# Performance work log

Measured on AMD Instinct MI355X. Metric: run time of the kernel, lower is better.

Reference implementation:

```python
import math
import jax, jax.numpy as jnp
import numpy as np

B, T, D_MODEL, H = 8, 2048, 1024, 16
D_HEAD = D_MODEL // H


def _rel_shift(x):
    # x: (B, T, H, H) -- faithful port of the TF pad/reshape/slice trick,
    # which in this module operates on the time axis (dim 1).
    b, t, h, h2 = x.shape
    x = jnp.pad(x, ((0, 0), (1, 0), (0, 0), (0, 0)))  # (B, T+1, H, H)
    x = x.reshape(t + 1, b, h, h2)[1:]                 # drop first row
    return x.reshape(b, t, h, h2)


def setup_inputs() -> dict:
    key = jax.random.key(0)
    ks = jax.random.split(key, 16)
    s = 1.0 / math.sqrt(D_MODEL)
    return {
        "inputs": jax.random.normal(ks[0], (B, T, D_MODEL), jnp.float32),
        "pos_embedding": jax.random.normal(ks[1], (B, T, D_MODEL), jnp.float32),
        "masks": jnp.ones((B, T), dtype=bool),
        "Wq": jax.random.normal(ks[2], (D_MODEL, D_MODEL), jnp.float32) * s,
        "bq": jnp.zeros((D_MODEL,), jnp.float32),
        "Wk": jax.random.normal(ks[3], (D_MODEL, D_MODEL), jnp.float32) * s,
        "bk": jnp.zeros((D_MODEL,), jnp.float32),
        "Wv": jax.random.normal(ks[4], (D_MODEL, D_MODEL), jnp.float32) * s,
        "bv": jnp.zeros((D_MODEL,), jnp.float32),
        "Wp": jax.random.normal(ks[5], (D_MODEL, D_MODEL), jnp.float32) * s,
        "Wo": jax.random.normal(ks[6], (D_MODEL, D_MODEL), jnp.float32) * s,
        "bo": jnp.zeros((D_MODEL,), jnp.float32),
        "u_bias": jax.random.normal(ks[7], (H, D_HEAD), jnp.float32) * 0.05,
        "v_bias": jax.random.normal(ks[8], (H, D_HEAD), jnp.float32) * 0.05,
    }


def reference(inputs, pos_embedding, masks, Wq, bq, Wk, bk, Wv, bv, Wp, Wo, bo, u_bias, v_bias):
    b, t, _ = inputs.shape
    sqrt_dim = math.sqrt(D_MODEL)
    q = (inputs @ Wq + bq).reshape(b, t, H, D_HEAD)
    k = (inputs @ Wk + bk).reshape(b, t, H, D_HEAD)
    v = (inputs @ Wv + bv).reshape(b, t, H, D_HEAD)
    p = (pos_embedding @ Wp).reshape(b, t, H, D_HEAD)

    # NOTE: no (B,H,T,D) transpose in the original -> HxH scores per timestep.
    content_score = jnp.einsum("bthd,btkd->bthk", q + u_bias, k)  # (B,T,H,H)
    pos_score = jnp.einsum("bthd,btkd->bthk", q + v_bias, p)      # (B,T,H,H)
    pos_score = _rel_shift(pos_score)
    score = (content_score + pos_score) / sqrt_dim
    score = jnp.where(masks[:, :, None, None], score, jnp.float32(1e-9))
    attn = jax.nn.softmax(score, axis=-1)
    ctx = jnp.einsum("bthk,btkd->bthd", attn, v)                  # (B,T,H,D)
    ctx = ctx.transpose(0, 2, 1, 3).reshape(b, -1, D_MODEL)       # (B,T,d_model)
    return ctx @ Wo + bo
```

## Files before the change

### kernel.cpp

```cpp
#include <hip/hip_runtime.h>


typedef __attribute__((ext_vector_type(8))) short short8;
typedef __attribute__((ext_vector_type(4))) float f32x4;

__device__ __forceinline__ ushort f2bf(float f) {
    unsigned u = __float_as_uint(f);
    u += 0x7FFFu + ((u >> 16) & 1u);
    return (ushort)(u >> 16);
}
__device__ __forceinline__ float bf2f(ushort u) {
    return __uint_as_float(((unsigned)u) << 16);
}

typedef const unsigned int __attribute__((address_space(1)))* gas_t;
typedef unsigned int __attribute__((address_space(3)))* las_t;
__device__ __forceinline__ void gl_lds16(const ushort* g, ushort* l) {
    __builtin_amdgcn_global_load_lds((gas_t)g, (las_t)l, 16, 0, 0);
}

__global__ __launch_bounds__(256)
void conv_bf16_k(const float* __restrict__ in, ushort* __restrict__ out)
{
    const size_t i = ((size_t)blockIdx.x * 256 + threadIdx.x) * 8;
    float4 a = *(const float4*)(in + i);
    float4 b = *(const float4*)(in + i + 4);
    short8 o = {(short)f2bf(a.x), (short)f2bf(a.y), (short)f2bf(a.z), (short)f2bf(a.w),
                (short)f2bf(b.x), (short)f2bf(b.y), (short)f2bf(b.z), (short)f2bf(b.w)};
    *(short8*)(out + i) = o;
}

__global__ __launch_bounds__(256)
void transpose_convert_k(const float* __restrict__ W, ushort* __restrict__ Wt, int K, int N)
{
    __shared__ float tile[32][33];
    const int tx = threadIdx.x & 31;
    const int ty = threadIdx.x >> 5;
    const int n0 = blockIdx.x * 32;
    const int k0 = blockIdx.y * 32;
#pragma unroll
    for (int i = 0; i < 4; ++i)
        tile[ty + i * 8][tx] = W[(size_t)(k0 + ty + i * 8) * N + n0 + tx];
    __syncthreads();
#pragma unroll
    for (int i = 0; i < 4; ++i)
        Wt[(size_t)(n0 + ty + i * 8) * K + k0 + tx] = f2bf(tile[tx][ty + i * 8]);
}

__global__ __launch_bounds__(256)
void bias_concat_k(const float* __restrict__ b0, const float* __restrict__ b1,
                   const float* __restrict__ b2, float* __restrict__ out)
{
    const int i = blockIdx.x * 256 + threadIdx.x;
    const int s = i >> 10;
    const int j = i & 1023;
    out[i] = (s == 0) ? b0[j] : (s == 1) ? b1[j] : b2[j];
}

#define VMC(n) asm volatile("s_waitcnt vmcnt(" #n ")" ::: "memory")

template<int HAS_BIAS, int OUT_BF16>
__global__ __launch_bounds__(512, 4)
void gemm6_k(const ushort* __restrict__ A, const ushort* __restrict__ Bt,
             const float* __restrict__ bias, void* __restrict__ Cv,
             int N, int K)
{
    __shared__ ushort As[3 * 4096];
    __shared__ ushort Bs[3 * 8192];
    const int tid = threadIdx.x;
    const int l = tid & 63;
    const int w = tid >> 6;
    const int wr = w >> 2;
    const int wc = w & 3;

    const int gx = gridDim.x;
    const int lin = blockIdx.y * gx + blockIdx.x;
    const int xcd = lin & 7;
    const int idx = lin >> 3;
    const int hb = gridDim.y >> 3;
    const int sxc = gx >> 2;
    const int g4 = idx >> 4;
    const int li = idx & 15;
    const int bx = (g4 % sxc) * 4 + (li & 3);
    const int by = xcd * hb + (g4 / sxc) * 4 + (li >> 2);
    const int bm = by * 128;
    const int bn = bx * 256;
    const int NT = K >> 5;

    const int srow = tid >> 2;
    const int scol = ((tid & 3) ^ ((tid >> 3) & 3)) * 8;
    const ushort* Ag  = A  + (size_t)(bm + srow) * K + scol;
    const ushort* Bg  = Bt + (size_t)(bn + srow) * K + scol;
    const ushort* Bg2 = Bg + (size_t)128 * K;
    const int lw = w * 512;

    const int lr = l & 15;
    const int fb = (((l >> 4) ^ ((l >> 1) & 3)) * 8);
    const int laneA = (wr * 64 + lr) * 32 + fb;
    const int laneB = (wc * 64 + lr) * 32 + fb;

    f32x4 acc[4][4];
#pragma unroll
    for (int i = 0; i < 4; ++i)
#pragma unroll
        for (int n = 0; n < 4; ++n)
            acc[i][n] = (f32x4){0.f, 0.f, 0.f, 0.f};

#define STAGE6(tt, rg) do { \
    ushort* ha = As + (rg) * 4096 + lw; \
    ushort* hbp = Bs + (rg) * 8192 + lw; \
    const size_t ko = (size_t)(tt) * 32; \
    gl_lds16(Ag + ko, ha); \
    gl_lds16(Bg + ko, hbp); \
    gl_lds16(Bg2 + ko, hbp + 4096); \
} while (0)

    STAGE6(0, 0);
    STAGE6(1, 1);
    VMC(3);
    __builtin_amdgcn_s_barrier();
    __builtin_amdgcn_sched_barrier(0);

    int cur = 0, stg = 2;
    for (int t = 0; t < NT; ++t) {
        if (t + 2 < NT) STAGE6(t + 2, stg);
        const ushort* ap = As + cur * 4096 + laneA;
        const ushort* bp = Bs + cur * 8192 + laneB;
        short8 af[4], bf4[4];
#pragma unroll
        for (int m = 0; m < 4; ++m) af[m] = *(const short8*)(ap + m * 512);
#pragma unroll
        for (int n = 0; n < 4; ++n) bf4[n] = *(const short8*)(bp + n * 512);
        asm volatile("s_waitcnt lgkmcnt(0)" ::: "memory");
        __builtin_amdgcn_sched_barrier(0);
        __builtin_amdgcn_s_setprio(1);
#pragma unroll
        for (int m = 0; m < 4; ++m)
#pragma unroll
            for (int n = 0; n < 4; ++n)
                acc[m][n] = __builtin_amdgcn_mfma_f32_16x16x32_bf16(af[m], bf4[n], acc[m][n], 0, 0, 0);
        __builtin_amdgcn_s_setprio(0);
        __builtin_amdgcn_sched_barrier(0);
        if (t < NT - 2) { VMC(3); }
        else if (t == NT - 2) { VMC(0); }
        if (t < NT - 1) {
            __builtin_amdgcn_s_barrier();
            __builtin_amdgcn_sched_barrier(0);
        }
        cur = (cur == 2) ? 0 : cur + 1;
        stg = (stg == 2) ? 0 : stg + 1;
    }
#undef STAGE6

    const int cr = (l >> 4) * 4;
    const int cc = l & 15;
    float bv[4];
#pragma unroll
    for (int n = 0; n < 4; ++n)
        bv[n] = HAS_BIAS ? bias[bn + wc * 64 + n * 16 + cc] : 0.f;
#pragma unroll
    for (int m = 0; m < 4; ++m) {
#pragma unroll
        for (int n = 0; n < 4; ++n) {
            const int col = bn + wc * 64 + n * 16 + cc;
#pragma unroll
            for (int r = 0; r < 4; ++r) {
                const int row = bm + wr * 64 + m * 16 + cr + r;
                float v = acc[m][n][r] + bv[n];
                if (OUT_BF16) ((ushort*)Cv)[(size_t)row * N + col] = f2bf(v);
                else          ((float*)Cv)[(size_t)row * N + col] = v;
            }
        }
    }
}

__global__ __launch_bounds__(256)
void attn2_k(const ushort* __restrict__ qkv, const ushort* __restrict__ pbuf,
             const float* __restrict__ ubias, const float* __restrict__ vbias,
             const int* __restrict__ masks, ushort* __restrict__ ctx)
{
    __shared__ __align__(16) float Pl[4][16 * 20];

    const int tid = threadIdx.x;
    const int w = tid >> 6;
    const int l = tid & 63;
    const int m = blockIdx.x * 4 + w;
    const int b2 = m >> 11;
    const int t2 = m & 2047;
    const int f  = m + 8;
    const int bs = f / 2049;
    const int ts = f - bs * 2049;
    const bool haspos = (ts != 0);
    const int mp = bs * 2048 + ts - 1;

    const int lr = l & 15;
    const int g  = l >> 4;
    const int ko = g * 8;

    const ushort* qb = qkv + (size_t)m * 3072;

    short8 quf[2], kf[2], qvf[2], pf[2];
#pragma unroll
    for (int c = 0; c < 2; ++c) {
        const int off = lr * 64 + c * 32 + ko;
        short8 q = *(const short8*)(qb + off);
        kf[c]    = *(const short8*)(qb + 1024 + off);
        float4 u0 = *(const float4*)(ubias + off);
        float4 u1 = *(const float4*)(ubias + off + 4);
        quf[c] = (short8){
            (short)f2bf(bf2f((ushort)q[0]) + u0.x), (short)f2bf(bf2f((ushort)q[1]) + u0.y),
            (short)f2bf(bf2f((ushort)q[2]) + u0.z), (short)f2bf(bf2f((ushort)q[3]) + u0.w),
            (short)f2bf(bf2f((ushort)q[4]) + u1.x), (short)f2bf(bf2f((ushort)q[5]) + u1.y),
            (short)f2bf(bf2f((ushort)q[6]) + u1.z), (short)f2bf(bf2f((ushort)q[7]) + u1.w)};
    }
    if (haspos) {
        const ushort* qmp = qkv + (size_t)mp * 3072;
        const ushort* pp  = pbuf + (size_t)mp * 1024;
#pragma unroll
        for (int c = 0; c < 2; ++c) {
            const int off = lr * 64 + c * 32 + ko;
            short8 q = *(const short8*)(qmp + off);
            pf[c]    = *(const short8*)(pp + off);
            float4 v0 = *(const float4*)(vbias + off);
            float4 v1 = *(const float4*)(vbias + off + 4);
            qvf[c] = (short8){
                (short)f2bf(bf2f((ushort)q[0]) + v0.x), (short)f2bf(bf2f((ushort)q[1]) + v0.y),
                (short)f2bf(bf2f((ushort)q[2]) + v0.z), (short)f2bf(bf2f((ushort)q[3]) + v0.w),
                (short)f2bf(bf2f((ushort)q[4]) + v1.x), (short)f2bf(bf2f((ushort)q[5]) + v1.y),
                (short)f2bf(bf2f((ushort)q[6]) + v1.z), (short)f2bf(bf2f((ushort)q[7]) + v1.w)};
        }
    }

    f32x4 s = (f32x4){0.f, 0.f, 0.f, 0.f};
    s = __builtin_amdgcn_mfma_f32_16x16x32_bf16(quf[0], kf[0], s, 0, 0, 0);
    s = __builtin_amdgcn_mfma_f32_16x16x32_bf16(quf[1], kf[1], s, 0, 0, 0);
    if (haspos) {
        s = __builtin_amdgcn_mfma_f32_16x16x32_bf16(qvf[0], pf[0], s, 0, 0, 0);
        s = __builtin_amdgcn_mfma_f32_16x16x32_bf16(qvf[1], pf[1], s, 0, 0, 0);
    }

    const bool mk = (masks[m] != 0);
    float sc[4];
#pragma unroll
    for (int r = 0; r < 4; ++r)
        sc[r] = mk ? s[r] * 0.03125f : 1e-9f;

    float mx[4], ex[4], sm[4];
#pragma unroll
    for (int r = 0; r < 4; ++r) {
        mx[r] = sc[r];
#pragma unroll
        for (int o = 8; o; o >>= 1) mx[r] = fmaxf(mx[r], __shfl_xor(mx[r], o, 64));
        ex[r] = __expf(sc[r] - mx[r]);
        sm[r] = ex[r];
#pragma unroll
        for (int o = 8; o; o >>= 1) sm[r] += __shfl_xor(sm[r], o, 64);
    }

    float* pw = Pl[w];
#pragma unroll
    for (int r = 0; r < 4; ++r)
        pw[(g * 4 + r) * 20 + lr] = ex[r] / sm[r];

    short8 pa;
    if (g < 2) {
        float4 p0 = *(const float4*)(pw + lr * 20 + g * 8);
        float4 p1 = *(const float4*)(pw + lr * 20 + g * 8 + 4);
        pa = (short8){(short)f2bf(p0.x), (short)f2bf(p0.y), (short)f2bf(p0.z), (short)f2bf(p0.w),
                      (short)f2bf(p1.x), (short)f2bf(p1.y), (short)f2bf(p1.z), (short)f2bf(p1.w)};
    } else {
        pa = (short8){0, 0, 0, 0, 0, 0, 0, 0};
    }

    const ushort* vb0 = qb + 2048;
    const size_t orow_base = (size_t)b2 * 2048 + (t2 >> 4);
    const int ocol_base = (t2 & 15) * 64;
#pragma unroll
    for (int n = 0; n < 4; ++n) {
        const int d0 = n * 16;
        short8 vf;
        if (g < 2) {
#pragma unroll
            for (int j = 0; j < 8; ++j)
                vf[j] = (short)vb0[(ko + j) * 64 + d0 + lr];
        } else {
            vf = (short8){0, 0, 0, 0, 0, 0, 0, 0};
        }
        f32x4 o = (f32x4){0.f, 0.f, 0.f, 0.f};
        o = __builtin_amdgcn_mfma_f32_16x16x32_bf16(pa, vf, o, 0, 0, 0);
#pragma unroll
        for (int r = 0; r < 4; ++r) {
            const int h1 = g * 4 + r;
            ctx[(orow_base + (size_t)h1 * 128) * 1024 + ocol_base + d0 + lr] = f2bf(o[r]);
        }
    }
}

extern "C" void kernel_launch(void* const* d_in, const int* in_sizes, int n_in,
                              void* d_out, int out_size, void* d_ws, size_t ws_size,
                              hipStream_t stream)
{
    (void)in_sizes; (void)n_in; (void)out_size; (void)ws_size;
    const float* inputs = (const float*)d_in[0];
    const float* pos    = (const float*)d_in[1];
    const int*   masks  = (const int*)d_in[2];
    const float* Wq = (const float*)d_in[3];
    const float* bq = (const float*)d_in[4];
    const float* Wk = (const float*)d_in[5];
    const float* bk = (const float*)d_in[6];
    const float* Wv = (const float*)d_in[7];
    const float* bv = (const float*)d_in[8];
    const float* Wp = (const float*)d_in[9];
    const float* Wo = (const float*)d_in[10];
    const float* bo = (const float*)d_in[11];
    const float* ub = (const float*)d_in[12];
    const float* vb = (const float*)d_in[13];

    char* ws = (char*)d_ws;
    const size_t WT_SZ = (size_t)1024 * 1024 * 2;
    ushort* WqT = (ushort*)(ws);
    ushort* WkT = (ushort*)(ws + 1 * WT_SZ);
    ushort* WvT = (ushort*)(ws + 2 * WT_SZ);
    ushort* WpT = (ushort*)(ws + 3 * WT_SZ);
    ushort* WoT = (ushort*)(ws + 4 * WT_SZ);
    float*  biascat = (float*)(ws + 5 * WT_SZ);
    char* bufs = ws + 5 * WT_SZ + 65536;
    const size_t S_SZ = (size_t)16384 * 1024 * 2;
    ushort* S1 = (ushort*)(bufs);
    ushort* S2 = (ushort*)(bufs + S_SZ);
    ushort* S3 = (ushort*)(bufs + 2 * S_SZ);

    dim3 blk(256);
    dim3 tgrid(32, 32);

    transpose_convert_k<<<tgrid, blk, 0, stream>>>(Wq, WqT, 1024, 1024);
    transpose_convert_k<<<tgrid, blk, 0, stream>>>(Wk, WkT, 1024, 1024);
    transpose_convert_k<<<tgrid, blk, 0, stream>>>(Wv, WvT, 1024, 1024);
    transpose_convert_k<<<tgrid, blk, 0, stream>>>(Wp, WpT, 1024, 1024);
    transpose_convert_k<<<tgrid, blk, 0, stream>>>(Wo, WoT, 1024, 1024);
    bias_concat_k<<<dim3(12), blk, 0, stream>>>(bq, bk, bv, biascat);

    conv_bf16_k<<<dim3(8192), blk, 0, stream>>>(pos, S1);
    gemm6_k<0, 1><<<dim3(4, 128), dim3(512), 0, stream>>>(S1, WpT, nullptr, S2, 1024, 1024);

    conv_bf16_k<<<dim3(8192), blk, 0, stream>>>(inputs, S1);
    gemm6_k<1, 1><<<dim3(12, 128), dim3(512), 0, stream>>>(S1, WqT, biascat, S3, 3072, 1024);

    attn2_k<<<dim3(4096), blk, 0, stream>>>(S3, S2, ub, vb, masks, S1);

    gemm6_k<1, 0><<<dim3(4, 128), dim3(512), 0, stream>>>(S1, WoT, bo, (float*)d_out, 1024, 1024);
}
```

Measured before the change: 290.5 us.

## Specialize GEMM to fixed K, fully unroll the loop and regroup barrier waits

The GEMM kernel now hardcodes K=1024 and fully unrolls the 32-step main loop, so buffer indices and wait counts become compile-time constants. The vmcnt wait and the workgroup barrier now run before the MFMA block instead of after it. The s_setprio raise around the MFMAs is removed. This cuts loop bookkeeping and scalar overhead. In exchange, code size grows, the kernel is tied to K=1024, and the earlier barrier may reduce overlap between the MFMAs and the in-flight global-to-LDS loads.

```diff
diff --git a/kernel.cpp b/kernel.cpp
--- a/kernel.cpp
+++ b/kernel.cpp
@@ -57,13 +57,15 @@
     out[i] = (s == 0) ? b0[j] : (s == 1) ? b1[j] : b2[j];
 }
 
+
 #define VMC(n) asm volatile("s_waitcnt vmcnt(" #n ")" ::: "memory")
+#define KDIM 1024
 
 template<int HAS_BIAS, int OUT_BF16>
 __global__ __launch_bounds__(512, 4)
-void gemm6_k(const ushort* __restrict__ A, const ushort* __restrict__ Bt,
+void gemm7_k(const ushort* __restrict__ A, const ushort* __restrict__ Bt,
              const float* __restrict__ bias, void* __restrict__ Cv,
-             int N, int K)
+             int N)
 {
     __shared__ ushort As[3 * 4096];
     __shared__ ushort Bs[3 * 8192];
@@ -85,13 +87,12 @@
     const int by = xcd * hb + (g4 / sxc) * 4 + (li >> 2);
     const int bm = by * 128;
     const int bn = bx * 256;
-    const int NT = K >> 5;
 
     const int srow = tid >> 2;
     const int scol = ((tid & 3) ^ ((tid >> 3) & 3)) * 8;
-    const ushort* Ag  = A  + (size_t)(bm + srow) * K + scol;
-    const ushort* Bg  = Bt + (size_t)(bn + srow) * K + scol;
-    const ushort* Bg2 = Bg + (size_t)128 * K;
+    const ushort* Ag  = A  + (size_t)(bm + srow) * KDIM + scol;
+    const ushort* Bg  = Bt + (size_t)(bn + srow) * KDIM + scol;
+    const ushort* Bg2 = Bg + (size_t)128 * KDIM;
     const int lw = w * 512;
 
     const int lr = l & 15;
@@ -106,7 +107,7 @@
         for (int n = 0; n < 4; ++n)
             acc[i][n] = (f32x4){0.f, 0.f, 0.f, 0.f};
 
-#define STAGE6(tt, rg) do { \
+#define STAGE7(tt, rg) do { \
     ushort* ha = As + (rg) * 4096 + lw; \
     ushort* hbp = Bs + (rg) * 8192 + lw; \
     const size_t ko = (size_t)(tt) * 32; \
@@ -115,15 +116,17 @@
     gl_lds16(Bg2 + ko, hbp + 4096); \
 } while (0)
 
-    STAGE6(0, 0);
-    STAGE6(1, 1);
+    STAGE7(0, 0);
+    STAGE7(1, 1);
     VMC(3);
     __builtin_amdgcn_s_barrier();
     __builtin_amdgcn_sched_barrier(0);
 
-    int cur = 0, stg = 2;
-    for (int t = 0; t < NT; ++t) {
-        if (t + 2 < NT) STAGE6(t + 2, stg);
+#pragma unroll
+    for (int t = 0; t < 32; ++t) {
+        const int cur = t % 3;
+        const int stg = (t + 2) % 3;
+        if (t + 2 < 32) STAGE7(t + 2, stg);
         const ushort* ap = As + cur * 4096 + laneA;
         const ushort* bp = Bs + cur * 8192 + laneB;
         short8 af[4], bf4[4];
@@ -131,26 +134,18 @@
         for (int m = 0; m < 4; ++m) af[m] = *(const short8*)(ap + m * 512);
 #pragma unroll
         for (int n = 0; n < 4; ++n) bf4[n] = *(const short8*)(bp + n * 512);
+        if (t < 30) { VMC(3); }
+        else if (t == 30) { VMC(0); }
         asm volatile("s_waitcnt lgkmcnt(0)" ::: "memory");
+        __builtin_amdgcn_s_barrier();
         __builtin_amdgcn_sched_barrier(0);
-        __builtin_amdgcn_s_setprio(1);
 #pragma unroll
         for (int m = 0; m < 4; ++m)
 #pragma unroll
             for (int n = 0; n < 4; ++n)
                 acc[m][n] = __builtin_amdgcn_mfma_f32_16x16x32_bf16(af[m], bf4[n], acc[m][n], 0, 0, 0);
-        __builtin_amdgcn_s_setprio(0);
-        __builtin_amdgcn_sched_barrier(0);
-        if (t < NT - 2) { VMC(3); }
-        else if (t == NT - 2) { VMC(0); }
-        if (t < NT - 1) {
-            __builtin_amdgcn_s_barrier();
-            __builtin_amdgcn_sched_barrier(0);
-        }
-        cur = (cur == 2) ? 0 : cur + 1;
-        stg = (stg == 2) ? 0 : stg + 1;
-    }
-#undef STAGE6
+    }
+#undef STAGE7
 
     const int cr = (l >> 4) * 4;
     const int cc = l & 15;
@@ -341,12 +336,12 @@
     bias_concat_k<<<dim3(12), blk, 0, stream>>>(bq, bk, bv, biascat);
 
     conv_bf16_k<<<dim3(8192), blk, 0, stream>>>(pos, S1);
-    gemm6_k<0, 1><<<dim3(4, 128), dim3(512), 0, stream>>>(S1, WpT, nullptr, S2, 1024, 1024);
+    gemm7_k<0, 1><<<dim3(4, 128), dim3(512), 0, stream>>>(S1, WpT, nullptr, S2, 1024);
 
     conv_bf16_k<<<dim3(8192), blk, 0, stream>>>(inputs, S1);
-    gemm6_k<1, 1><<<dim3(12, 128), dim3(512), 0, stream>>>(S1, WqT, biascat, S3, 3072, 1024);
+    gemm7_k<1, 1><<<dim3(12, 128), dim3(512), 0, stream>>>(S1, WqT, biascat, S3, 3072);
 
     attn2_k<<<dim3(4096), blk, 0, stream>>>(S3, S2, ub, vb, masks, S1);
 
-    gemm6_k<1, 0><<<dim3(4, 128), dim3(512), 0, stream>>>(S1, WoT, bo, (float*)d_out, 1024, 1024);
-}
+    gemm7_k<1, 0><<<dim3(4, 128), dim3(512), 0, stream>>>(S1, WoT, bo, (float*)d_out, 1024);
+}
```

Result: no change. 286.3 us (-1.4%).
